# Kernel tuning notes

Hardware: AMD Instinct MI355X
Metric: run time of the kernel (lower is better)

## Reference

```python
import jax, jax.numpy as jnp
import numpy as np

NUM_NODES = 2048      # nodes per graph
N = 65536             # total nodes = 16 pairs * 2 graphs * 2048
E = 524288            # total edges
D = 128               # node_state_dim
ED = 64               # edge_encoded_dim
H = 256               # message_hidden_dim
M = 128               # message_dim
U = 256               # update_hidden_dim


def _mlp3(x, W1, b1, W2, b2, W3, b3):
    h = jax.nn.relu(x @ W1 + b1)
    h = jax.nn.relu(h @ W2 + b2)
    return h @ W3 + b3


def setup_inputs() -> dict:
    key = jax.random.key(0)
    ks = jax.random.split(key, 16)
    s = 0.02
    inp = {
        "node_states": jax.random.normal(ks[0], (N, D), jnp.float32),
        "edges": jax.random.normal(ks[1], (E, ED), jnp.float32),
        "vertices": jax.random.randint(ks[2], (E, 2), 0, N, jnp.int32),
        # message_encoder params
        "mW1": jax.random.normal(ks[3], (2 * D + ED, H), jnp.float32) * s,
        "mb1": jnp.zeros((H,), jnp.float32),
        "mW2": jax.random.normal(ks[4], (H, H), jnp.float32) * s,
        "mb2": jnp.zeros((H,), jnp.float32),
        "mW3": jax.random.normal(ks[5], (H, M), jnp.float32) * s,
        "mb3": jnp.zeros((M,), jnp.float32),
        # node_update params
        "uW1": jax.random.normal(ks[6], (D + M + D, U), jnp.float32) * s,
        "ub1": jnp.zeros((U,), jnp.float32),
        "uW2": jax.random.normal(ks[7], (U, U), jnp.float32) * s,
        "ub2": jnp.zeros((U,), jnp.float32),
        "uW3": jax.random.normal(ks[8], (U, D), jnp.float32) * s,
        "ub3": jnp.zeros((D,), jnp.float32),
    }
    return inp


def reference(node_states, edges, vertices,
              mW1, mb1, mW2, mb2, mW3, mb3,
              uW1, ub1, uW2, ub2, uW3, ub3):
    # gather endpoint states: [E, D] each
    nodes_i = node_states[vertices[:, 0]]
    nodes_j = node_states[vertices[:, 1]]
    # message MLP on [E, 2D+ED]
    messages = _mlp3(jnp.concatenate([nodes_i, nodes_j, edges], axis=1),
                     mW1, mb1, mW2, mb2, mW3, mb3)
    # scatter-add each message to BOTH endpoints (torch code repeats messages
    # twice and scatters by [v0; v1; arange] with zero padding for all nodes)
    summed = (jax.ops.segment_sum(messages, vertices[:, 0], num_segments=N)
              + jax.ops.segment_sum(messages, vertices[:, 1], num_segments=N))
    # cross-graph attention vectors: pairs of graphs, difference both ways
    paired = node_states.reshape(-1, 2, NUM_NODES, D)
    attention = jnp.concatenate([paired[:, 0] - paired[:, 1],
                                 paired[:, 1] - paired[:, 0]], axis=1).reshape(-1, D)
    upd_in = jnp.concatenate([node_states, summed, attention], axis=1)
    return _mlp3(upd_in, uW1, ub1, uW2, ub2, uW3, ub3)
```

## Files before the change

### kernel.cpp

```cpp
#include <hip/hip_runtime.h>

#define NNODES 65536
#define NEDGES 524288

typedef short bf16x8 __attribute__((ext_vector_type(8)));
typedef float f32x4 __attribute__((ext_vector_type(4)));

#define OF_MW1 0
#define OF_MW2 81920
#define OF_MW3 147456
#define OF_UW1 180224
#define OF_UW2 278528
#define OF_UW3 344064
#define WF_BYTES (376832 * 2)

#define WS_MSGS_BYTES ((size_t)NEDGES * 128 * 2)
#define WS_EIDX_OFF   WS_MSGS_BYTES
#define WS_EIDX_BYTES ((size_t)NNODES * 64 * 4)
#define WS_CNT_OFF    (WS_EIDX_OFF + WS_EIDX_BYTES)
#define WS_CNT_BYTES  ((size_t)NNODES * 4)
#define WS_WF_OFF     (WS_CNT_OFF + WS_CNT_BYTES)
#define WS_NEED       (WS_WF_OFF + WF_BYTES)

#define WS_SUMMED_BYTES ((size_t)NNODES * 128 * 4)

__device__ __forceinline__ unsigned short f2bf(float x) {
  unsigned int u = __float_as_uint(x);
  return (unsigned short)((u + 0x7FFFu + ((u >> 16) & 1u)) >> 16);
}

__device__ __forceinline__ float bf2f(short s) {
  return __uint_as_float((unsigned int)(unsigned short)s << 16);
}

__device__ __forceinline__ void cvt_store8(unsigned short* p, float4 a, float4 b) {
  union { unsigned short u[8]; bf16x8 v; } t;
  t.u[0] = f2bf(a.x); t.u[1] = f2bf(a.y); t.u[2] = f2bf(a.z); t.u[3] = f2bf(a.w);
  t.u[4] = f2bf(b.x); t.u[5] = f2bf(b.y); t.u[6] = f2bf(b.z); t.u[7] = f2bf(b.w);
  *reinterpret_cast<bf16x8*>(p) = t.v;
}

template <int KT, int NTW>
__device__ __forceinline__ void gemm_tile64(const unsigned short* A, const int lda,
                                            const unsigned short* Wf,
                                            f32x4 (&acc)[4][NTW], const int lane) {
  const int ar = lane & 15;
  const int ak = (lane >> 4) << 3;
#pragma unroll
  for (int kt = 0; kt < KT; ++kt) {
    bf16x8 a[4];
#pragma unroll
    for (int m = 0; m < 4; ++m)
      a[m] = *reinterpret_cast<const bf16x8*>(&A[(m * 16 + ar) * lda + kt * 32 + ak]);
#pragma unroll
    for (int n = 0; n < NTW; ++n) {
      bf16x8 b = *reinterpret_cast<const bf16x8*>(&Wf[(n * KT + kt) * 512 + lane * 8]);
#pragma unroll
      for (int m = 0; m < 4; ++m)
        acc[m][n] = __builtin_amdgcn_mfma_f32_16x16x32_bf16(a[m], b, acc[m][n], 0, 0, 0);
    }
  }
}

__global__ void prep_weights(const float* __restrict__ mW1, const float* __restrict__ mW2,
                             const float* __restrict__ mW3, const float* __restrict__ uW1,
                             const float* __restrict__ uW2, const float* __restrict__ uW3,
                             unsigned short* __restrict__ wf) {
  const int f = blockIdx.x;
  const int lane = threadIdx.x;
  const float* W; int NC, KT, fl, base;
  if (f < 160)      { W = mW1; NC = 256; KT = 10; fl = f;       base = OF_MW1; }
  else if (f < 288) { W = mW2; NC = 256; KT = 8;  fl = f - 160; base = OF_MW2; }
  else if (f < 352) { W = mW3; NC = 128; KT = 8;  fl = f - 288; base = OF_MW3; }
  else if (f < 544) { W = uW1; NC = 256; KT = 12; fl = f - 352; base = OF_UW1; }
  else if (f < 672) { W = uW2; NC = 256; KT = 8;  fl = f - 544; base = OF_UW2; }
  else              { W = uW3; NC = 128; KT = 8;  fl = f - 672; base = OF_UW3; }
  const int n_t = fl / KT;
  const int k_t = fl % KT;
  const int col = n_t * 16 + (lane & 15);
  const int krow = k_t * 32 + ((lane >> 4) << 3);
  unsigned short* dst = wf + base + (size_t)fl * 512 + lane * 8;
#pragma unroll
  for (int e = 0; e < 8; ++e) dst[e] = f2bf(W[(size_t)(krow + e) * NC + col]);
}

__global__ void fill_csr(const int* __restrict__ verts, int* __restrict__ cnt,
                         int* __restrict__ eidx) {
  const int k = blockIdx.x * 256 + threadIdx.x;
  const int v = verts[k];
  const int slot = atomicAdd(&cnt[v], 1);
  if (slot < 64) eidx[(size_t)v * 64 + slot] = k >> 1;
}

template <bool ATOMIC>
__global__ __launch_bounds__(256, 3) void msg_kernel(
    const float* __restrict__ ns, const float* __restrict__ edg,
    const int* __restrict__ verts, const unsigned short* __restrict__ wf,
    const float* __restrict__ mb1, const float* __restrict__ mb2,
    const float* __restrict__ mb3, float* __restrict__ summed,
    unsigned short* __restrict__ msgs) {
  extern __shared__ unsigned short smem[];
  unsigned short* Xs = smem;
  int* vl = (int*)(smem + 64 * 328);

  const int tid = threadIdx.x;
  const int lane = tid & 63;
  const int w = tid >> 6;
  const int e0 = blockIdx.x * 64;

  if (tid < 128) vl[tid] = verts[(size_t)e0 * 2 + tid];
#pragma unroll
  for (int i = tid; i < 512; i += 256) {
    const int row = i >> 3;
    const int c = (i & 7) * 8;
    const float4* s2 = reinterpret_cast<const float4*>(edg + (size_t)(e0 + row) * 64 + c);
    cvt_store8(&Xs[row * 328 + 256 + c], s2[0], s2[1]);
  }
  __syncthreads();

  {
    const int r = tid >> 4;
    const int c = (tid & 15) * 8;
#pragma unroll
    for (int p = 0; p < 4; ++p) {
      const int row = p * 16 + r;
      const float4* s0 = reinterpret_cast<const float4*>(ns + (size_t)vl[2 * row] * 128 + c);
      cvt_store8(&Xs[row * 328 + c], s0[0], s0[1]);
      const float4* s1 = reinterpret_cast<const float4*>(ns + (size_t)vl[2 * row + 1] * 128 + c);
      cvt_store8(&Xs[row * 328 + 128 + c], s1[0], s1[1]);
    }
  }
  __syncthreads();

  const int cw = lane & 15;
  const int rq = (lane >> 4) * 4;

  {
    f32x4 acc[4][4];
#pragma unroll
    for (int m = 0; m < 4; ++m)
#pragma unroll
      for (int n = 0; n < 4; ++n)
#pragma unroll
        for (int i = 0; i < 4; ++i) acc[m][n][i] = 0.0f;
    gemm_tile64<10, 4>(Xs, 328, wf + OF_MW1 + (size_t)(w * 4) * 10 * 512, acc, lane);
    __syncthreads();
#pragma unroll
    for (int n = 0; n < 4; ++n) {
      const int col = w * 64 + n * 16 + cw;
      const float bias = mb1[col];
#pragma unroll
      for (int m = 0; m < 4; ++m)
#pragma unroll
        for (int q = 0; q < 4; ++q) {
          const int row = m * 16 + rq + q;
          Xs[row * 328 + col] = f2bf(fmaxf(acc[m][n][q] + bias, 0.0f));
        }
    }
  }
  __syncthreads();

  {
    f32x4 acc[4][4];
#pragma unroll
    for (int m = 0; m < 4; ++m)
#pragma unroll
      for (int n = 0; n < 4; ++n)
#pragma unroll
        for (int i = 0; i < 4; ++i) acc[m][n][i] = 0.0f;
    gemm_tile64<8, 4>(Xs, 328, wf + OF_MW2 + (size_t)(w * 4) * 8 * 512, acc, lane);
    __syncthreads();
#pragma unroll
    for (int n = 0; n < 4; ++n) {
      const int col = w * 64 + n * 16 + cw;
      const float bias = mb2[col];
#pragma unroll
      for (int m = 0; m < 4; ++m)
#pragma unroll
        for (int q = 0; q < 4; ++q) {
          const int row = m * 16 + rq + q;
          Xs[row * 328 + col] = f2bf(fmaxf(acc[m][n][q] + bias, 0.0f));
        }
    }
  }
  __syncthreads();

  {
    f32x4 acc[4][2];
#pragma unroll
    for (int m = 0; m < 4; ++m)
#pragma unroll
      for (int n = 0; n < 2; ++n)
#pragma unroll
        for (int i = 0; i < 4; ++i) acc[m][n][i] = 0.0f;
    gemm_tile64<8, 2>(Xs, 328, wf + OF_MW3 + (size_t)(w * 2) * 8 * 512, acc, lane);

    if constexpr (ATOMIC) {
#pragma unroll
      for (int n = 0; n < 2; ++n) {
        const int col = w * 32 + n * 16 + cw;
        const float bias = mb3[col];
#pragma unroll
        for (int m = 0; m < 4; ++m)
#pragma unroll
          for (int q = 0; q < 4; ++q) {
            const int row = m * 16 + rq + q;
            const float v = acc[m][n][q] + bias;
            unsafeAtomicAdd(&summed[(size_t)vl[2 * row] * 128 + col], v);
            unsafeAtomicAdd(&summed[(size_t)vl[2 * row + 1] * 128 + col], v);
          }
      }
    } else {
      __syncthreads();
#pragma unroll
      for (int n = 0; n < 2; ++n) {
        const int col = w * 32 + n * 16 + cw;
        const float bias = mb3[col];
#pragma unroll
        for (int m = 0; m < 4; ++m)
#pragma unroll
          for (int q = 0; q < 4; ++q) {
            const int row = m * 16 + rq + q;
            Xs[row * 328 + col] = f2bf(acc[m][n][q] + bias);
          }
      }
      __syncthreads();
#pragma unroll
      for (int i = tid; i < 1024; i += 256) {
        const int row = i >> 4;
        const int c = (i & 15) * 8;
        *reinterpret_cast<bf16x8*>(&msgs[(size_t)(e0 + row) * 128 + c]) =
            *reinterpret_cast<const bf16x8*>(&Xs[row * 328 + c]);
      }
    }
  }
}

template <bool GATHER>
__global__ __launch_bounds__(256, 3) void upd_kernel(
    const float* __restrict__ ns, const float* __restrict__ summed,
    const unsigned short* __restrict__ msgs, const int* __restrict__ cnt,
    const int* __restrict__ eidx, const unsigned short* __restrict__ wf,
    const float* __restrict__ ub1, const float* __restrict__ ub2,
    const float* __restrict__ ub3, float* __restrict__ out) {
  extern __shared__ unsigned short smem[];
  unsigned short* Xs = smem;

  const int tid = threadIdx.x;
  const int lane = tid & 63;
  const int w = tid >> 6;
  const int n0 = blockIdx.x * 64;

  for (int i = tid; i < 1024; i += 256) {
    const int row = i >> 4;
    const int c = (i & 15) * 8;
    const int n = n0 + row;
    const float4* sA = reinterpret_cast<const float4*>(ns + (size_t)n * 128 + c);
    const float4 a0 = sA[0], a1 = sA[1];
    cvt_store8(&Xs[row * 392 + c], a0, a1);
    if constexpr (!GATHER) {
      const float4* sS = reinterpret_cast<const float4*>(summed + (size_t)n * 128 + c);
      cvt_store8(&Xs[row * 392 + 128 + c], sS[0], sS[1]);
    }
    const float4* sP = reinterpret_cast<const float4*>(ns + (size_t)(n ^ 2048) * 128 + c);
    const float4 p0 = sP[0], p1 = sP[1];
    float4 d0, d1;
    d0.x = a0.x - p0.x; d0.y = a0.y - p0.y; d0.z = a0.z - p0.z; d0.w = a0.w - p0.w;
    d1.x = a1.x - p1.x; d1.y = a1.y - p1.y; d1.z = a1.z - p1.z; d1.w = a1.w - p1.w;
    cvt_store8(&Xs[row * 392 + 256 + c], d0, d1);
  }

  if constexpr (GATHER) {
    for (int i = tid; i < 1024; i += 256) {
      const int row = i >> 4;
      const int q4 = i & 15;
      reinterpret_cast<int4*>(&Xs[row * 392 + 128])[q4] =
          reinterpret_cast<const int4*>(&eidx[(size_t)(n0 + row) * 64])[q4];
    }
    __syncthreads();

    const int nl = tid >> 2;
    const int part = tid & 3;
    const int cn = min(cnt[n0 + nl], 64);
    const int* el = reinterpret_cast<const int*>(&Xs[nl * 392 + 128]);
    float acc[32];
#pragma unroll
    for (int k = 0; k < 32; ++k) acc[k] = 0.0f;
    for (int j = 0; j < cn; ++j) {
      const int e = el[j];
      const bf16x8* mp = reinterpret_cast<const bf16x8*>(&msgs[(size_t)e * 128 + part * 32]);
#pragma unroll
      for (int t = 0; t < 4; ++t) {
        const bf16x8 v = mp[t];
#pragma unroll
        for (int k = 0; k < 8; ++k) acc[t * 8 + k] += bf2f(v[k]);
      }
    }
    __syncthreads();
#pragma unroll
    for (int t = 0; t < 4; ++t) {
      union { unsigned short u[8]; bf16x8 v; } o;
#pragma unroll
      for (int k = 0; k < 8; ++k) o.u[k] = f2bf(acc[t * 8 + k]);
      *reinterpret_cast<bf16x8*>(&Xs[nl * 392 + 128 + part * 32 + t * 8]) = o.v;
    }
  }
  __syncthreads();

  const int cw = lane & 15;
  const int rq = (lane >> 4) * 4;

  {
    f32x4 acc[4][4];
#pragma unroll
    for (int m = 0; m < 4; ++m)
#pragma unroll
      for (int n = 0; n < 4; ++n)
#pragma unroll
        for (int i = 0; i < 4; ++i) acc[m][n][i] = 0.0f;
    gemm_tile64<12, 4>(Xs, 392, wf + OF_UW1 + (size_t)(w * 4) * 12 * 512, acc, lane);
    __syncthreads();
#pragma unroll
    for (int n = 0; n < 4; ++n) {
      const int col = w * 64 + n * 16 + cw;
      const float bias = ub1[col];
#pragma unroll
      for (int m = 0; m < 4; ++m)
#pragma unroll
        for (int q = 0; q < 4; ++q) {
          const int row = m * 16 + rq + q;
          Xs[row * 392 + col] = f2bf(fmaxf(acc[m][n][q] + bias, 0.0f));
        }
    }
  }
  __syncthreads();

  {
    f32x4 acc[4][4];
#pragma unroll
    for (int m = 0; m < 4; ++m)
#pragma unroll
      for (int n = 0; n < 4; ++n)
#pragma unroll
        for (int i = 0; i < 4; ++i) acc[m][n][i] = 0.0f;
    gemm_tile64<8, 4>(Xs, 392, wf + OF_UW2 + (size_t)(w * 4) * 8 * 512, acc, lane);
    __syncthreads();
#pragma unroll
    for (int n = 0; n < 4; ++n) {
      const int col = w * 64 + n * 16 + cw;
      const float bias = ub2[col];
#pragma unroll
      for (int m = 0; m < 4; ++m)
#pragma unroll
        for (int q = 0; q < 4; ++q) {
          const int row = m * 16 + rq + q;
          Xs[row * 392 + col] = f2bf(fmaxf(acc[m][n][q] + bias, 0.0f));
        }
    }
  }
  __syncthreads();

  {
    f32x4 acc[4][2];
#pragma unroll
    for (int m = 0; m < 4; ++m)
#pragma unroll
      for (int n = 0; n < 2; ++n)
#pragma unroll
        for (int i = 0; i < 4; ++i) acc[m][n][i] = 0.0f;
    gemm_tile64<8, 2>(Xs, 392, wf + OF_UW3 + (size_t)(w * 2) * 8 * 512, acc, lane);
#pragma unroll
    for (int n = 0; n < 2; ++n) {
      const int col = w * 32 + n * 16 + cw;
      const float bias = ub3[col];
#pragma unroll
      for (int m = 0; m < 4; ++m)
#pragma unroll
        for (int q = 0; q < 4; ++q) {
          const int row = m * 16 + rq + q;
          out[(size_t)(n0 + row) * 128 + col] = acc[m][n][q] + bias;
        }
    }
  }
}

extern "C" void kernel_launch(void* const* d_in, const int* in_sizes, int n_in,
                              void* d_out, int out_size, void* d_ws, size_t ws_size,
                              hipStream_t stream) {
  const float* ns   = (const float*)d_in[0];
  const float* edg  = (const float*)d_in[1];
  const int* verts  = (const int*)d_in[2];
  const float* mW1  = (const float*)d_in[3];
  const float* mb1  = (const float*)d_in[4];
  const float* mW2  = (const float*)d_in[5];
  const float* mb2  = (const float*)d_in[6];
  const float* mW3  = (const float*)d_in[7];
  const float* mb3  = (const float*)d_in[8];
  const float* uW1  = (const float*)d_in[9];
  const float* ub1  = (const float*)d_in[10];
  const float* uW2  = (const float*)d_in[11];
  const float* ub2  = (const float*)d_in[12];
  const float* uW3  = (const float*)d_in[13];
  const float* ub3  = (const float*)d_in[14];
  float* out = (float*)d_out;

  const int msg_lds = 64 * 328 * 2 + 128 * 4;
  const int upd_lds = 64 * 392 * 2;

  if (ws_size >= WS_NEED) {
    unsigned short* msgs = (unsigned short*)d_ws;
    int* eidx = (int*)((char*)d_ws + WS_EIDX_OFF);
    int* cnt  = (int*)((char*)d_ws + WS_CNT_OFF);
    unsigned short* wf = (unsigned short*)((char*)d_ws + WS_WF_OFF);

    hipMemsetAsync(cnt, 0, WS_CNT_BYTES, stream);
    prep_weights<<<736, 64, 0, stream>>>(mW1, mW2, mW3, uW1, uW2, uW3, wf);
    fill_csr<<<2 * NEDGES / 256, 256, 0, stream>>>(verts, cnt, eidx);
    msg_kernel<false><<<NEDGES / 64, 256, msg_lds, stream>>>(
        ns, edg, verts, wf, mb1, mb2, mb3, nullptr, msgs);
    upd_kernel<true><<<NNODES / 64, 256, upd_lds, stream>>>(
        ns, nullptr, msgs, cnt, eidx, wf, ub1, ub2, ub3, out);
  } else {
    float* summed = (float*)d_ws;
    unsigned short* wf = (unsigned short*)((char*)d_ws + WS_SUMMED_BYTES);

    hipMemsetAsync(summed, 0, WS_SUMMED_BYTES, stream);
    prep_weights<<<736, 64, 0, stream>>>(mW1, mW2, mW3, uW1, uW2, uW3, wf);
    msg_kernel<true><<<NEDGES / 64, 256, msg_lds, stream>>>(
        ns, edg, verts, wf, mb1, mb2, mb3, summed, nullptr);
    upd_kernel<false><<<NNODES / 64, 256, upd_lds, stream>>>(
        ns, summed, nullptr, nullptr, nullptr, wf, ub1, ub2, ub3, out);
  }
}
```

Before: 559.9 us.

## Stream gathered inputs directly into first MLP GEMM with 2-wave blocks

Result: slower. 849.2 us (+51.7%).

```diff
diff --git a/kernel.cpp b/kernel.cpp
--- a/kernel.cpp
+++ b/kernel.cpp
@@ -33,11 +33,15 @@
   return __uint_as_float((unsigned int)(unsigned short)s << 16);
 }
 
-__device__ __forceinline__ void cvt_store8(unsigned short* p, float4 a, float4 b) {
+__device__ __forceinline__ bf16x8 pack8(float4 a, float4 b) {
   union { unsigned short u[8]; bf16x8 v; } t;
   t.u[0] = f2bf(a.x); t.u[1] = f2bf(a.y); t.u[2] = f2bf(a.z); t.u[3] = f2bf(a.w);
   t.u[4] = f2bf(b.x); t.u[5] = f2bf(b.y); t.u[6] = f2bf(b.z); t.u[7] = f2bf(b.w);
-  *reinterpret_cast<bf16x8*>(p) = t.v;
+  return t.v;
+}
+
+__device__ __forceinline__ void cvt_store8(unsigned short* p, float4 a, float4 b) {
+  *reinterpret_cast<bf16x8*>(p) = pack8(a, b);
 }
 
 template <int KT, int NTW>
@@ -93,119 +97,120 @@
 }
 
 template <bool ATOMIC>
-__global__ __launch_bounds__(256, 3) void msg_kernel(
+__global__ __launch_bounds__(128, 2) void msg_kernel(
     const float* __restrict__ ns, const float* __restrict__ edg,
     const int* __restrict__ verts, const unsigned short* __restrict__ wf,
     const float* __restrict__ mb1, const float* __restrict__ mb2,
     const float* __restrict__ mb3, float* __restrict__ summed,
     unsigned short* __restrict__ msgs) {
   extern __shared__ unsigned short smem[];
-  unsigned short* Xs = smem;
-  int* vl = (int*)(smem + 64 * 328);
+  unsigned short* H = smem;
+  int* vl = (int*)(smem + 64 * 264);
 
   const int tid = threadIdx.x;
   const int lane = tid & 63;
   const int w = tid >> 6;
   const int e0 = blockIdx.x * 64;
 
-  if (tid < 128) vl[tid] = verts[(size_t)e0 * 2 + tid];
-#pragma unroll
-  for (int i = tid; i < 512; i += 256) {
-    const int row = i >> 3;
-    const int c = (i & 7) * 8;
-    const float4* s2 = reinterpret_cast<const float4*>(edg + (size_t)(e0 + row) * 64 + c);
-    cvt_store8(&Xs[row * 328 + 256 + c], s2[0], s2[1]);
-  }
-  __syncthreads();
-
-  {
-    const int r = tid >> 4;
-    const int c = (tid & 15) * 8;
-#pragma unroll
-    for (int p = 0; p < 4; ++p) {
-      const int row = p * 16 + r;
-      const float4* s0 = reinterpret_cast<const float4*>(ns + (size_t)vl[2 * row] * 128 + c);
-      cvt_store8(&Xs[row * 328 + c], s0[0], s0[1]);
-      const float4* s1 = reinterpret_cast<const float4*>(ns + (size_t)vl[2 * row + 1] * 128 + c);
-      cvt_store8(&Xs[row * 328 + 128 + c], s1[0], s1[1]);
-    }
-  }
-  __syncthreads();
-
+  vl[tid] = verts[(size_t)e0 * 2 + tid];
+  __syncthreads();
+
+  const int er = lane & 15;
+  const int ak = (lane >> 4) << 3;
   const int cw = lane & 15;
   const int rq = (lane >> 4) * 4;
+  int vi[4], vj[4];
+#pragma unroll
+  for (int m = 0; m < 4; ++m) {
+    vi[m] = vl[2 * (m * 16 + er)];
+    vj[m] = vl[2 * (m * 16 + er) + 1];
+  }
+
+  f32x4 acc[4][8];
+#pragma unroll
+  for (int m = 0; m < 4; ++m)
+#pragma unroll
+    for (int n = 0; n < 8; ++n)
+#pragma unroll
+      for (int i = 0; i < 4; ++i) acc[m][n][i] = 0.0f;
+
+#pragma unroll
+  for (int kt = 0; kt < 10; ++kt) {
+    bf16x8 a[4];
+#pragma unroll
+    for (int m = 0; m < 4; ++m) {
+      const float* src;
+      if (kt < 4)      src = ns + (size_t)vi[m] * 128 + kt * 32 + ak;
+      else if (kt < 8) src = ns + (size_t)vj[m] * 128 + (kt - 4) * 32 + ak;
+      else             src = edg + (size_t)(e0 + m * 16 + er) * 64 + (kt - 8) * 32 + ak;
+      const float4* s = reinterpret_cast<const float4*>(src);
+      a[m] = pack8(s[0], s[1]);
+    }
+#pragma unroll
+    for (int n = 0; n < 8; ++n) {
+      bf16x8 b = *reinterpret_cast<const bf16x8*>(
+          &wf[OF_MW1 + ((size_t)(w * 8 + n) * 10 + kt) * 512 + lane * 8]);
+#pragma unroll
+      for (int m = 0; m < 4; ++m)
+        acc[m][n] = __builtin_amdgcn_mfma_f32_16x16x32_bf16(a[m], b, acc[m][n], 0, 0, 0);
+    }
+  }
+#pragma unroll
+  for (int n = 0; n < 8; ++n) {
+    const int col = w * 128 + n * 16 + cw;
+    const float bias = mb1[col];
+#pragma unroll
+    for (int m = 0; m < 4; ++m)
+#pragma unroll
+      for (int q = 0; q < 4; ++q)
+        H[(m * 16 + rq + q) * 264 + col] = f2bf(fmaxf(acc[m][n][q] + bias, 0.0f));
+  }
+  __syncthreads();
 
   {
-    f32x4 acc[4][4];
+    f32x4 acc2[4][8];
+#pragma unroll
+    for (int m = 0; m < 4; ++m)
+#pragma unroll
+      for (int n = 0; n < 8; ++n)
+#pragma unroll
+        for (int i = 0; i < 4; ++i) acc2[m][n][i] = 0.0f;
+    gemm_tile64<8, 8>(H, 264, wf + OF_MW2 + (size_t)(w * 8) * 8 * 512, acc2, lane);
+    __syncthreads();
+#pragma unroll
+    for (int n = 0; n < 8; ++n) {
+      const int col = w * 128 + n * 16 + cw;
+      const float bias = mb2[col];
+#pragma unroll
+      for (int m = 0; m < 4; ++m)
+#pragma unroll
+        for (int q = 0; q < 4; ++q)
+          H[(m * 16 + rq + q) * 264 + col] = f2bf(fmaxf(acc2[m][n][q] + bias, 0.0f));
+    }
+  }
+  __syncthreads();
+
+  {
+    f32x4 acc3[4][4];
 #pragma unroll
     for (int m = 0; m < 4; ++m)
 #pragma unroll
       for (int n = 0; n < 4; ++n)
 #pragma unroll
-        for (int i = 0; i < 4; ++i) acc[m][n][i] = 0.0f;
-    gemm_tile64<10, 4>(Xs, 328, wf + OF_MW1 + (size_t)(w * 4) * 10 * 512, acc, lane);
-    __syncthreads();
-#pragma unroll
-    for (int n = 0; n < 4; ++n) {
-      const int col = w * 64 + n * 16 + cw;
-      const float bias = mb1[col];
-#pragma unroll
-      for (int m = 0; m < 4; ++m)
-#pragma unroll
-        for (int q = 0; q < 4; ++q) {
-          const int row = m * 16 + rq + q;
-          Xs[row * 328 + col] = f2bf(fmaxf(acc[m][n][q] + bias, 0.0f));
-        }
-    }
-  }
-  __syncthreads();
-
-  {
-    f32x4 acc[4][4];
-#pragma unroll
-    for (int m = 0; m < 4; ++m)
-#pragma unroll
-      for (int n = 0; n < 4; ++n)
-#pragma unroll
-        for (int i = 0; i < 4; ++i) acc[m][n][i] = 0.0f;
-    gemm_tile64<8, 4>(Xs, 328, wf + OF_MW2 + (size_t)(w * 4) * 8 * 512, acc, lane);
-    __syncthreads();
-#pragma unroll
-    for (int n = 0; n < 4; ++n) {
-      const int col = w * 64 + n * 16 + cw;
-      const float bias = mb2[col];
-#pragma unroll
-      for (int m = 0; m < 4; ++m)
-#pragma unroll
-        for (int q = 0; q < 4; ++q) {
-          const int row = m * 16 + rq + q;
-          Xs[row * 328 + col] = f2bf(fmaxf(acc[m][n][q] + bias, 0.0f));
-        }
-    }
-  }
-  __syncthreads();
-
-  {
-    f32x4 acc[4][2];
-#pragma unroll
-    for (int m = 0; m < 4; ++m)
-#pragma unroll
-      for (int n = 0; n < 2; ++n)
-#pragma unroll
-        for (int i = 0; i < 4; ++i) acc[m][n][i] = 0.0f;
-    gemm_tile64<8, 2>(Xs, 328, wf + OF_MW3 + (size_t)(w * 2) * 8 * 512, acc, lane);
+        for (int i = 0; i < 4; ++i) acc3[m][n][i] = 0.0f;
+    gemm_tile64<8, 4>(H, 264, wf + OF_MW3 + (size_t)(w * 4) * 8 * 512, acc3, lane);
 
     if constexpr (ATOMIC) {
 #pragma unroll
-      for (int n = 0; n < 2; ++n) {
-        const int col = w * 32 + n * 16 + cw;
+      for (int n = 0; n < 4; ++n) {
+        const int col = w * 64 + n * 16 + cw;
         const float bias = mb3[col];
 #pragma unroll
         for (int m = 0; m < 4; ++m)
 #pragma unroll
           for (int q = 0; q < 4; ++q) {
             const int row = m * 16 + rq + q;
-            const float v = acc[m][n][q] + bias;
+            const float v = acc3[m][n][q] + bias;
             unsafeAtomicAdd(&summed[(size_t)vl[2 * row] * 128 + col], v);
             unsafeAtomicAdd(&summed[(size_t)vl[2 * row + 1] * 128 + col], v);
           }
@@ -213,25 +218,22 @@
     } else {
       __syncthreads();
 #pragma unroll
-      for (int n = 0; n < 2; ++n) {
-        const int col = w * 32 + n * 16 + cw;
+      for (int n = 0; n < 4; ++n) {
+        const int col = w * 64 + n * 16 + cw;
         const float bias = mb3[col];
 #pragma unroll
         for (int m = 0; m < 4; ++m)
 #pragma unroll
-          for (int q = 0; q < 4; ++q) {
-            const int row = m * 16 + rq + q;
-            Xs[row * 328 + col] = f2bf(acc[m][n][q] + bias);
-          }
+          for (int q = 0; q < 4; ++q)
+            H[(m * 16 + rq + q) * 264 + col] = f2bf(acc3[m][n][q] + bias);
       }
       __syncthreads();
-#pragma unroll
-      for (int i = tid; i < 1024; i += 256) {
-        const int row = i >> 4;
-        const int c = (i & 15) * 8;
-        *reinterpret_cast<bf16x8*>(&msgs[(size_t)(e0 + row) * 128 + c]) =
-            *reinterpret_cast<const bf16x8*>(&Xs[row * 328 + c]);
-      }
+      const int row = tid >> 1;
+      const int ch = (tid & 1) * 64;
+#pragma unroll
+      for (int j = 0; j < 8; ++j)
+        *reinterpret_cast<bf16x8*>(&msgs[(size_t)(e0 + row) * 128 + ch + j * 8]) =
+            *reinterpret_cast<const bf16x8*>(&H[row * 264 + ch + j * 8]);
     }
   }
 }
@@ -404,7 +406,7 @@
   const float* ub3  = (const float*)d_in[14];
   float* out = (float*)d_out;
 
-  const int msg_lds = 64 * 328 * 2 + 128 * 4;
+  const int msg_lds = 64 * 264 * 2 + 128 * 4;
   const int upd_lds = 64 * 392 * 2;
 
   if (ws_size >= WS_NEED) {
@@ -413,10 +415,10 @@
     int* cnt  = (int*)((char*)d_ws + WS_CNT_OFF);
     unsigned short* wf = (unsigned short*)((char*)d_ws + WS_WF_OFF);
 
-    hipMemsetAsync(cnt, 0, WS_CNT_BYTES, stream);
+    (void)hipMemsetAsync(cnt, 0, WS_CNT_BYTES, stream);
     prep_weights<<<736, 64, 0, stream>>>(mW1, mW2, mW3, uW1, uW2, uW3, wf);
     fill_csr<<<2 * NEDGES / 256, 256, 0, stream>>>(verts, cnt, eidx);
-    msg_kernel<false><<<NEDGES / 64, 256, msg_lds, stream>>>(
+    msg_kernel<false><<<NEDGES / 64, 128, msg_lds, stream>>>(
         ns, edg, verts, wf, mb1, mb2, mb3, nullptr, msgs);
     upd_kernel<true><<<NNODES / 64, 256, upd_lds, stream>>>(
         ns, nullptr, msgs, cnt, eidx, wf, ub1, ub2, ub3, out);
@@ -424,9 +426,9 @@
     float* summed = (float*)d_ws;
     unsigned short* wf = (unsigned short*)((char*)d_ws + WS_SUMMED_BYTES);
 
-    hipMemsetAsync(summed, 0, WS_SUMMED_BYTES, stream);
+    (void)hipMemsetAsync(summed, 0, WS_SUMMED_BYTES, stream);
     prep_weights<<<736, 64, 0, stream>>>(mW1, mW2, mW3, uW1, uW2, uW3, wf);
-    msg_kernel<true><<<NEDGES / 64, 256, msg_lds, stream>>>(
+    msg_kernel<true><<<NEDGES / 64, 128, msg_lds, stream>>>(
         ns, edg, verts, wf, mb1, mb2, mb3, summed, nullptr);
     upd_kernel<false><<<NNODES / 64, 256, upd_lds, stream>>>(
         ns, summed, nullptr, nullptr, nullptr, wf, ub1, ub2, ub3, out);
```

## Software-pipeline MFMA operand loads and retile update kernel to 32-row blocks

Applied to the files above, without the earlier changes.

Result: no change. 556.2 us (-0.7%).

```diff
diff --git a/kernel.cpp b/kernel.cpp
--- a/kernel.cpp
+++ b/kernel.cpp
@@ -40,24 +40,42 @@
   *reinterpret_cast<bf16x8*>(p) = t.v;
 }
 
-template <int KT, int NTW>
-__device__ __forceinline__ void gemm_tile64(const unsigned short* A, const int lda,
-                                            const unsigned short* Wf,
-                                            f32x4 (&acc)[4][NTW], const int lane) {
+template <int MT, int KT, int NTW>
+__device__ __forceinline__ void gemm_tile(const unsigned short* A, const int lda,
+                                          const unsigned short* Wf,
+                                          f32x4 (&acc)[MT][NTW], const int lane) {
   const int ar = lane & 15;
   const int ak = (lane >> 4) << 3;
+  bf16x8 bcur[NTW], acur[MT];
+#pragma unroll
+  for (int n = 0; n < NTW; ++n)
+    bcur[n] = *reinterpret_cast<const bf16x8*>(&Wf[(size_t)(n * KT) * 512 + lane * 8]);
+#pragma unroll
+  for (int m = 0; m < MT; ++m)
+    acur[m] = *reinterpret_cast<const bf16x8*>(&A[(m * 16 + ar) * lda + ak]);
 #pragma unroll
   for (int kt = 0; kt < KT; ++kt) {
-    bf16x8 a[4];
-#pragma unroll
-    for (int m = 0; m < 4; ++m)
-      a[m] = *reinterpret_cast<const bf16x8*>(&A[(m * 16 + ar) * lda + kt * 32 + ak]);
-#pragma unroll
-    for (int n = 0; n < NTW; ++n) {
-      bf16x8 b = *reinterpret_cast<const bf16x8*>(&Wf[(n * KT + kt) * 512 + lane * 8]);
-#pragma unroll
-      for (int m = 0; m < 4; ++m)
-        acc[m][n] = __builtin_amdgcn_mfma_f32_16x16x32_bf16(a[m], b, acc[m][n], 0, 0, 0);
+    bf16x8 bnxt[NTW], anxt[MT];
+    if (kt + 1 < KT) {
+#pragma unroll
+      for (int n = 0; n < NTW; ++n)
+        bnxt[n] = *reinterpret_cast<const bf16x8*>(
+            &Wf[(size_t)(n * KT + kt + 1) * 512 + lane * 8]);
+#pragma unroll
+      for (int m = 0; m < MT; ++m)
+        anxt[m] = *reinterpret_cast<const bf16x8*>(
+            &A[(m * 16 + ar) * lda + (kt + 1) * 32 + ak]);
+    }
+#pragma unroll
+    for (int n = 0; n < NTW; ++n)
+#pragma unroll
+      for (int m = 0; m < MT; ++m)
+        acc[m][n] = __builtin_amdgcn_mfma_f32_16x16x32_bf16(acur[m], bcur[n], acc[m][n], 0, 0, 0);
+    if (kt + 1 < KT) {
+#pragma unroll
+      for (int n = 0; n < NTW; ++n) bcur[n] = bnxt[n];
+#pragma unroll
+      for (int m = 0; m < MT; ++m) acur[m] = anxt[m];
     }
   }
 }
@@ -143,7 +161,7 @@
       for (int n = 0; n < 4; ++n)
 #pragma unroll
         for (int i = 0; i < 4; ++i) acc[m][n][i] = 0.0f;
-    gemm_tile64<10, 4>(Xs, 328, wf + OF_MW1 + (size_t)(w * 4) * 10 * 512, acc, lane);
+    gemm_tile<4, 10, 4>(Xs, 328, wf + OF_MW1 + (size_t)(w * 4) * 10 * 512, acc, lane);
     __syncthreads();
 #pragma unroll
     for (int n = 0; n < 4; ++n) {
@@ -168,7 +186,7 @@
       for (int n = 0; n < 4; ++n)
 #pragma unroll
         for (int i = 0; i < 4; ++i) acc[m][n][i] = 0.0f;
-    gemm_tile64<8, 4>(Xs, 328, wf + OF_MW2 + (size_t)(w * 4) * 8 * 512, acc, lane);
+    gemm_tile<4, 8, 4>(Xs, 328, wf + OF_MW2 + (size_t)(w * 4) * 8 * 512, acc, lane);
     __syncthreads();
 #pragma unroll
     for (int n = 0; n < 4; ++n) {
@@ -193,7 +211,7 @@
       for (int n = 0; n < 2; ++n)
 #pragma unroll
         for (int i = 0; i < 4; ++i) acc[m][n][i] = 0.0f;
-    gemm_tile64<8, 2>(Xs, 328, wf + OF_MW3 + (size_t)(w * 2) * 8 * 512, acc, lane);
+    gemm_tile<4, 8, 2>(Xs, 328, wf + OF_MW3 + (size_t)(w * 2) * 8 * 512, acc, lane);
 
     if constexpr (ATOMIC) {
 #pragma unroll
@@ -237,7 +255,7 @@
 }
 
 template <bool GATHER>
-__global__ __launch_bounds__(256, 3) void upd_kernel(
+__global__ __launch_bounds__(128, 3) void upd_kernel(
     const float* __restrict__ ns, const float* __restrict__ summed,
     const unsigned short* __restrict__ msgs, const int* __restrict__ cnt,
     const int* __restrict__ eidx, const unsigned short* __restrict__ wf,
@@ -249,9 +267,9 @@
   const int tid = threadIdx.x;
   const int lane = tid & 63;
   const int w = tid >> 6;
-  const int n0 = blockIdx.x * 64;
-
-  for (int i = tid; i < 1024; i += 256) {
+  const int n0 = blockIdx.x * 32;
+
+  for (int i = tid; i < 512; i += 128) {
     const int row = i >> 4;
     const int c = (i & 15) * 8;
     const int n = n0 + row;
@@ -271,7 +289,7 @@
   }
 
   if constexpr (GATHER) {
-    for (int i = tid; i < 1024; i += 256) {
+    for (int i = tid; i < 512; i += 128) {
       const int row = i >> 4;
       const int q4 = i & 15;
       reinterpret_cast<int4*>(&Xs[row * 392 + 128])[q4] =
@@ -311,21 +329,21 @@
   const int rq = (lane >> 4) * 4;
 
   {
-    f32x4 acc[4][4];
-#pragma unroll
-    for (int m = 0; m < 4; ++m)
-#pragma unroll
-      for (int n = 0; n < 4; ++n)
-#pragma unroll
-        for (int i = 0; i < 4; ++i) acc[m][n][i] = 0.0f;
-    gemm_tile64<12, 4>(Xs, 392, wf + OF_UW1 + (size_t)(w * 4) * 12 * 512, acc, lane);
-    __syncthreads();
-#pragma unroll
-    for (int n = 0; n < 4; ++n) {
-      const int col = w * 64 + n * 16 + cw;
+    f32x4 acc[2][8];
+#pragma unroll
+    for (int m = 0; m < 2; ++m)
+#pragma unroll
+      for (int n = 0; n < 8; ++n)
+#pragma unroll
+        for (int i = 0; i < 4; ++i) acc[m][n][i] = 0.0f;
+    gemm_tile<2, 12, 8>(Xs, 392, wf + OF_UW1 + (size_t)(w * 8) * 12 * 512, acc, lane);
+    __syncthreads();
+#pragma unroll
+    for (int n = 0; n < 8; ++n) {
+      const int col = w * 128 + n * 16 + cw;
       const float bias = ub1[col];
 #pragma unroll
-      for (int m = 0; m < 4; ++m)
+      for (int m = 0; m < 2; ++m)
 #pragma unroll
         for (int q = 0; q < 4; ++q) {
           const int row = m * 16 + rq + q;
@@ -336,21 +354,21 @@
   __syncthreads();
 
   {
-    f32x4 acc[4][4];
-#pragma unroll
-    for (int m = 0; m < 4; ++m)
-#pragma unroll
-      for (int n = 0; n < 4; ++n)
-#pragma unroll
-        for (int i = 0; i < 4; ++i) acc[m][n][i] = 0.0f;
-    gemm_tile64<8, 4>(Xs, 392, wf + OF_UW2 + (size_t)(w * 4) * 8 * 512, acc, lane);
-    __syncthreads();
-#pragma unroll
-    for (int n = 0; n < 4; ++n) {
-      const int col = w * 64 + n * 16 + cw;
+    f32x4 acc[2][8];
+#pragma unroll
+    for (int m = 0; m < 2; ++m)
+#pragma unroll
+      for (int n = 0; n < 8; ++n)
+#pragma unroll
+        for (int i = 0; i < 4; ++i) acc[m][n][i] = 0.0f;
+    gemm_tile<2, 8, 8>(Xs, 392, wf + OF_UW2 + (size_t)(w * 8) * 8 * 512, acc, lane);
+    __syncthreads();
+#pragma unroll
+    for (int n = 0; n < 8; ++n) {
+      const int col = w * 128 + n * 16 + cw;
       const float bias = ub2[col];
 #pragma unroll
-      for (int m = 0; m < 4; ++m)
+      for (int m = 0; m < 2; ++m)
 #pragma unroll
         for (int q = 0; q < 4; ++q) {
           const int row = m * 16 + rq + q;
@@ -361,20 +379,20 @@
   __syncthreads();
 
   {
-    f32x4 acc[4][2];
-#pragma unroll
-    for (int m = 0; m < 4; ++m)
-#pragma unroll
-      for (int n = 0; n < 2; ++n)
-#pragma unroll
-        for (int i = 0; i < 4; ++i) acc[m][n][i] = 0.0f;
-    gemm_tile64<8, 2>(Xs, 392, wf + OF_UW3 + (size_t)(w * 2) * 8 * 512, acc, lane);
-#pragma unroll
-    for (int n = 0; n < 2; ++n) {
-      const int col = w * 32 + n * 16 + cw;
+    f32x4 acc[2][4];
+#pragma unroll
+    for (int m = 0; m < 2; ++m)
+#pragma unroll
+      for (int n = 0; n < 4; ++n)
+#pragma unroll
+        for (int i = 0; i < 4; ++i) acc[m][n][i] = 0.0f;
+    gemm_tile<2, 8, 4>(Xs, 392, wf + OF_UW3 + (size_t)(w * 4) * 8 * 512, acc, lane);
+#pragma unroll
+    for (int n = 0; n < 4; ++n) {
+      const int col = w * 64 + n * 16 + cw;
       const float bias = ub3[col];
 #pragma unroll
-      for (int m = 0; m < 4; ++m)
+      for (int m = 0; m < 2; ++m)
 #pragma unroll
         for (int q = 0; q < 4; ++q) {
           const int row = m * 16 + rq + q;
@@ -405,7 +423,7 @@
   float* out = (float*)d_out;
 
   const int msg_lds = 64 * 328 * 2 + 128 * 4;
-  const int upd_lds = 64 * 392 * 2;
+  const int upd_lds = 32 * 392 * 2;
 
   if (ws_size >= WS_NEED) {
     unsigned short* msgs = (unsigned short*)d_ws;
@@ -413,22 +431,22 @@
     int* cnt  = (int*)((char*)d_ws + WS_CNT_OFF);
     unsigned short* wf = (unsigned short*)((char*)d_ws + WS_WF_OFF);
 
-    hipMemsetAsync(cnt, 0, WS_CNT_BYTES, stream);
+    (void)hipMemsetAsync(cnt, 0, WS_CNT_BYTES, stream);
     prep_weights<<<736, 64, 0, stream>>>(mW1, mW2, mW3, uW1, uW2, uW3, wf);
     fill_csr<<<2 * NEDGES / 256, 256, 0, stream>>>(verts, cnt, eidx);
     msg_kernel<false><<<NEDGES / 64, 256, msg_lds, stream>>>(
         ns, edg, verts, wf, mb1, mb2, mb3, nullptr, msgs);
-    upd_kernel<true><<<NNODES / 64, 256, upd_lds, stream>>>(
+    upd_kernel<true><<<NNODES / 32, 128, upd_lds, stream>>>(
         ns, nullptr, msgs, cnt, eidx, wf, ub1, ub2, ub3, out);
   } else {
     float* summed = (float*)d_ws;
     unsigned short* wf = (unsigned short*)((char*)d_ws + WS_SUMMED_BYTES);
 
-    hipMemsetAsync(summed, 0, WS_SUMMED_BYTES, stream);
+    (void)hipMemsetAsync(summed, 0, WS_SUMMED_BYTES, stream);
     prep_weights<<<736, 64, 0, stream>>>(mW1, mW2, mW3, uW1, uW2, uW3, wf);
     msg_kernel<true><<<NEDGES / 64, 256, msg_lds, stream>>>(
         ns, edg, verts, wf, mb1, mb2, mb3, summed, nullptr);
-    upd_kernel<false><<<NNODES / 64, 256, upd_lds, stream>>>(
+    upd_kernel<false><<<NNODES / 32, 128, upd_lds, stream>>>(
         ns, summed, nullptr, nullptr, nullptr, wf, ub1, ub2, ub3, out);
   }
 }
```
